# Performance work log

Measured on AMD Instinct MI355X. Metric: run time of the kernel, lower is better.

## Reference

```python
import jax, jax.numpy as jnp
import numpy as np

N, D = 16384, 2048

def setup_inputs() -> dict:
    key = jax.random.key(0)
    k1, k2, k3 = jax.random.split(key, 3)
    x1 = jax.random.normal(k1, (N, D), dtype=jnp.float32)
    x2 = jax.random.normal(k2, (N, D), dtype=jnp.float32)
    w = jax.random.normal(k3, (D,), dtype=jnp.float32)
    return {"x1": x1, "x2": x2, "w": w}

def reference(x1, x2, w):
    # per-row attention scores: s_k[i] = dot(x_k[i], w)
    s1 = x1 @ w  # [N]
    s2 = x2 @ w  # [N]
    # alpha_1 = exp(s1)/(exp(s1)+exp(s2)) == sigmoid(s1 - s2) (numerically stable)
    alpha1 = jax.nn.sigmoid(s1 - s2)  # [N]
    alpha2 = 1.0 - alpha1
    fused = alpha1[:, None] * x1 + alpha2[:, None] * x2  # [N, D]
    alpha = jnp.stack([alpha1, alpha2], axis=1)  # [N, 2], detached in original
    return fused, alpha
```

## Files before the change

### kernel.cpp

```cpp
#include <hip/hip_runtime.h>


#define NROWS 16384
#define DCOLS 2048

__global__ __launch_bounds__(256) void attn_fuse_kernel(
    const float* __restrict__ x1,
    const float* __restrict__ x2,
    const float* __restrict__ w,
    float* __restrict__ fused,
    float* __restrict__ alpha)
{
    const int row = blockIdx.x;
    const int t = threadIdx.x;

    const float4* x1v = (const float4*)(x1 + (size_t)row * DCOLS);
    const float4* x2v = (const float4*)(x2 + (size_t)row * DCOLS);
    const float4* wv  = (const float4*)w;

    float4 a0 = x1v[t];
    float4 a1 = x1v[t + 256];
    float4 b0 = x2v[t];
    float4 b1 = x2v[t + 256];
    float4 w0 = wv[t];
    float4 w1 = wv[t + 256];

    float p = (a0.x - b0.x) * w0.x + (a0.y - b0.y) * w0.y
            + (a0.z - b0.z) * w0.z + (a0.w - b0.w) * w0.w
            + (a1.x - b1.x) * w1.x + (a1.y - b1.y) * w1.y
            + (a1.z - b1.z) * w1.z + (a1.w - b1.w) * w1.w;

    #pragma unroll
    for (int off = 32; off > 0; off >>= 1)
        p += __shfl_down(p, off, 64);

    __shared__ float wave_sum[4];
    const int wave = t >> 6;
    const int lane = t & 63;
    if (lane == 0) wave_sum[wave] = p;
    __syncthreads();
    const float d = wave_sum[0] + wave_sum[1] + wave_sum[2] + wave_sum[3];

    const float a1g = 1.0f / (1.0f + expf(-d));

    float4 f0, f1;
    f0.x = b0.x + a1g * (a0.x - b0.x);
    f0.y = b0.y + a1g * (a0.y - b0.y);
    f0.z = b0.z + a1g * (a0.z - b0.z);
    f0.w = b0.w + a1g * (a0.w - b0.w);
    f1.x = b1.x + a1g * (a1.x - b1.x);
    f1.y = b1.y + a1g * (a1.y - b1.y);
    f1.z = b1.z + a1g * (a1.z - b1.z);
    f1.w = b1.w + a1g * (a1.w - b1.w);

    float4* outv = (float4*)(fused + (size_t)row * DCOLS);
    outv[t] = f0;
    outv[t + 256] = f1;

    if (t == 0) {
        alpha[(size_t)row * 2]     = a1g;
        alpha[(size_t)row * 2 + 1] = 1.0f - a1g;
    }
}

extern "C" void kernel_launch(void* const* d_in, const int* in_sizes, int n_in,
                              void* d_out, int out_size, void* d_ws, size_t ws_size,
                              hipStream_t stream)
{
    const float* x1 = (const float*)d_in[0];
    const float* x2 = (const float*)d_in[1];
    const float* w  = (const float*)d_in[2];

    float* fused = (float*)d_out;
    float* alpha = fused + (size_t)NROWS * DCOLS;

    attn_fuse_kernel<<<NROWS, 256, 0, stream>>>(x1, x2, w, fused, alpha);
}
```

Baseline: 307.1 us.

## Process one row per wavefront with nontemporal stores, removing block sync

```diff
diff --git a/kernel.cpp b/kernel.cpp
--- a/kernel.cpp
+++ b/kernel.cpp
@@ -3,63 +3,59 @@
 
 #define NROWS 16384
 #define DCOLS 2048
+#define WPB 4
 
-__global__ __launch_bounds__(256) void attn_fuse_kernel(
+typedef float vfloat4 __attribute__((ext_vector_type(4)));
+typedef float vfloat2 __attribute__((ext_vector_type(2)));
+
+__global__ __launch_bounds__(256) void attn_fuse_wave(
     const float* __restrict__ x1,
     const float* __restrict__ x2,
     const float* __restrict__ w,
     float* __restrict__ fused,
     float* __restrict__ alpha)
 {
-    const int row = blockIdx.x;
-    const int t = threadIdx.x;
+    const int wave = threadIdx.x >> 6;
+    const int lane = threadIdx.x & 63;
+    const int row  = blockIdx.x * WPB + wave;
 
-    const float4* x1v = (const float4*)(x1 + (size_t)row * DCOLS);
-    const float4* x2v = (const float4*)(x2 + (size_t)row * DCOLS);
-    const float4* wv  = (const float4*)w;
+    const vfloat4* __restrict__ x1v = (const vfloat4*)(x1 + (size_t)row * DCOLS);
+    const vfloat4* __restrict__ x2v = (const vfloat4*)(x2 + (size_t)row * DCOLS);
+    const vfloat4* __restrict__ wv  = (const vfloat4*)w;
 
-    float4 a0 = x1v[t];
-    float4 a1 = x1v[t + 256];
-    float4 b0 = x2v[t];
-    float4 b1 = x2v[t + 256];
-    float4 w0 = wv[t];
-    float4 w1 = wv[t + 256];
+    vfloat4 a[8], b[8], wr[8];
+    #pragma unroll
+    for (int j = 0; j < 8; ++j) a[j]  = x1v[lane + 64 * j];
+    #pragma unroll
+    for (int j = 0; j < 8; ++j) b[j]  = x2v[lane + 64 * j];
+    #pragma unroll
+    for (int j = 0; j < 8; ++j) wr[j] = wv[lane + 64 * j];
 
-    float p = (a0.x - b0.x) * w0.x + (a0.y - b0.y) * w0.y
-            + (a0.z - b0.z) * w0.z + (a0.w - b0.w) * w0.w
-            + (a1.x - b1.x) * w1.x + (a1.y - b1.y) * w1.y
-            + (a1.z - b1.z) * w1.z + (a1.w - b1.w) * w1.w;
+    float p = 0.0f;
+    #pragma unroll
+    for (int j = 0; j < 8; ++j) {
+        vfloat4 d = (a[j] - b[j]) * wr[j];
+        p += d.x + d.y + d.z + d.w;
+    }
 
     #pragma unroll
-    for (int off = 32; off > 0; off >>= 1)
-        p += __shfl_down(p, off, 64);
+    for (int off = 1; off < 64; off <<= 1)
+        p += __shfl_xor(p, off, 64);
 
-    __shared__ float wave_sum[4];
-    const int wave = t >> 6;
-    const int lane = t & 63;
-    if (lane == 0) wave_sum[wave] = p;
-    __syncthreads();
-    const float d = wave_sum[0] + wave_sum[1] + wave_sum[2] + wave_sum[3];
+    const float g = 1.0f / (1.0f + expf(-p));
 
-    const float a1g = 1.0f / (1.0f + expf(-d));
+    vfloat4* outv = (vfloat4*)(fused + (size_t)row * DCOLS);
+    #pragma unroll
+    for (int j = 0; j < 8; ++j) {
+        vfloat4 f = b[j] + g * (a[j] - b[j]);
+        __builtin_nontemporal_store(f, &outv[lane + 64 * j]);
+    }
 
-    float4 f0, f1;
-    f0.x = b0.x + a1g * (a0.x - b0.x);
-    f0.y = b0.y + a1g * (a0.y - b0.y);
-    f0.z = b0.z + a1g * (a0.z - b0.z);
-    f0.w = b0.w + a1g * (a0.w - b0.w);
-    f1.x = b1.x + a1g * (a1.x - b1.x);
-    f1.y = b1.y + a1g * (a1.y - b1.y);
-    f1.z = b1.z + a1g * (a1.z - b1.z);
-    f1.w = b1.w + a1g * (a1.w - b1.w);
-
-    float4* outv = (float4*)(fused + (size_t)row * DCOLS);
-    outv[t] = f0;
-    outv[t + 256] = f1;
-
-    if (t == 0) {
-        alpha[(size_t)row * 2]     = a1g;
-        alpha[(size_t)row * 2 + 1] = 1.0f - a1g;
+    if (lane == 0) {
+        vfloat2 al;
+        al.x = g;
+        al.y = 1.0f - g;
+        __builtin_nontemporal_store(al, (vfloat2*)(alpha + (size_t)row * 2));
     }
 }
 
@@ -74,5 +70,5 @@
     float* fused = (float*)d_out;
     float* alpha = fused + (size_t)NROWS * DCOLS;
 
-    attn_fuse_kernel<<<NROWS, 256, 0, stream>>>(x1, x2, w, fused, alpha);
+    attn_fuse_wave<<<NROWS / WPB, 256, 0, stream>>>(x1, x2, w, fused, alpha);
 }
```

Measured after the change: 326.2 us. 1.06x slower.
